# Performance work log

Measured on AMD Instinct MI355X. Metric: run time of the kernel, lower is better.

## Reference

```python
import jax, jax.numpy as jnp
import numpy as np

B, K, T, H, D = 16, 49, 256, 512, 512


def setup_inputs() -> dict:
    key = jax.random.key(0)
    ks = jax.random.split(key, 8)
    s = 1.0 / np.sqrt(H)
    return {
        "V": jax.random.normal(ks[0], (B, K, H), jnp.float32),
        "h_t": jax.random.normal(ks[1], (B, T, H), jnp.float32),
        "s_t": jax.random.normal(ks[2], (B, T, H), jnp.float32),
        "Wv": jax.random.normal(ks[3], (H, D), jnp.float32) * s,
        "bv": jnp.zeros((D,), jnp.float32),
        "Wg": jax.random.normal(ks[4], (H, D), jnp.float32) * s,
        "bg": jnp.zeros((D,), jnp.float32),
        "Ws": jax.random.normal(ks[5], (H, D), jnp.float32) * s,
        "bs": jnp.zeros((D,), jnp.float32),
        "Wh": jax.random.normal(ks[6], (D, 1), jnp.float32) * (1.0 / np.sqrt(D)),
        "bh": jnp.zeros((1,), jnp.float32),
    }


def reference(V, h_t, s_t, Wv, bv, Wg, bg, Ws, bs, Wh, bh):
    # projections (dropout is identity in eval)
    cv = V @ Wv + bv                        # [B, K, D]
    cg = h_t @ Wg + bg                      # [B, T, D]
    # content_v: [B, T, K, D] via broadcast add
    content_v = cv[:, None, :, :] + cg[:, :, None, :]
    z_t = (jnp.tanh(content_v) @ Wh + bh)[..., 0]   # [B, T, K]
    alpha_t = jax.nn.softmax(z_t, axis=-1)          # [B, T, K]
    c_t = jnp.einsum('btk,bkh->bth', alpha_t, V)    # [B, T, H]
    # sentinel branch
    content_s = (s_t @ Ws + bs) + cg                # [B, T, D]
    z_ext = jnp.tanh(content_s) @ Wh + bh           # [B, T, 1]
    extended = jnp.concatenate([z_t, z_ext], axis=-1)  # [B, T, K+1]
    alpha_hat = jax.nn.softmax(extended, axis=-1)
    beta_t = alpha_hat[:, :, -1:]                   # [B, T, 1]
    c_hat_t = beta_t * s_t + (1.0 - beta_t) * c_t   # [B, T, H]
    return (c_hat_t, alpha_t, beta_t)
```

## Files before the change

kernel.cpp:

```cpp
#include <hip/hip_runtime.h>
#include <hip/hip_fp16.h>
#include <cstdint>
#include <cstddef>

#define B_ 16
#define K_ 49
#define T_ 256
#define H_ 512
#define D_ 512

#define TANH_SCALE 2.8853900817779268f
#define LOG2E 1.4426950408889634f

typedef _Float16 half8 __attribute__((ext_vector_type(8)));
typedef float floatx4 __attribute__((ext_vector_type(4)));

#define ROWS_A 9088
#define OFF_V 0
#define OFF_H 896
#define OFF_S 4992

__device__ __forceinline__ void async16(const _Float16* g, const _Float16* l) {
    __builtin_amdgcn_global_load_lds(
        (const __attribute__((address_space(1))) unsigned int*)g,
        (__attribute__((address_space(3))) unsigned int*)l, 16, 0, 0);
}

__global__ __launch_bounds__(256) void conv_all(const float* __restrict__ V,
                                                const float* __restrict__ h_t,
                                                const float* __restrict__ s_t,
                                                const float* __restrict__ Wv,
                                                const float* __restrict__ Wg,
                                                const float* __restrict__ Ws,
                                                _Float16* __restrict__ Af16,
                                                _Float16* __restrict__ Wt) {
    __shared__ float tile[32][33];
    int tid = threadIdx.x;
    if (blockIdx.x < 2272) {
        int idx = (blockIdx.x * 256 + tid) * 8;
        int row = idx >> 9;
        int col = idx & 511;
        const float* src;
        if (row < 784)        src = V   + (size_t)row * 512 + col;
        else if (row < 896)   src = nullptr;
        else if (row < 4992)  src = h_t + (size_t)(row - 896) * 512 + col;
        else                  src = s_t + (size_t)(row - 4992) * 512 + col;
        half8 h;
        if (src) {
            float4 f0 = *(const float4*)(src);
            float4 f1 = *(const float4*)(src + 4);
            h[0] = (_Float16)f0.x; h[1] = (_Float16)f0.y;
            h[2] = (_Float16)f0.z; h[3] = (_Float16)f0.w;
            h[4] = (_Float16)f1.x; h[5] = (_Float16)f1.y;
            h[6] = (_Float16)f1.z; h[7] = (_Float16)f1.w;
        } else {
            h = (half8)((_Float16)0.0f);
        }
        *(half8*)(Af16 + idx) = h;
    } else {
        int bid = blockIdx.x - 2272;
        int p = bid >> 8;
        int rem = bid & 255;
        int bx = rem & 15, by = rem >> 4;
        const float* W = (p == 0) ? Wv : (p == 1) ? Wg : Ws;
        _Float16* outp = Wt + (size_t)p * 512 * 512;
        int tx = tid & 31, ty = tid >> 5;
        int c = bx * 32 + tx;
        int rbase = by * 32;
#pragma unroll
        for (int i = 0; i < 4; i++)
            tile[ty + i * 8][tx] = W[(size_t)(rbase + ty + i * 8) * 512 + c];
        __syncthreads();
        int k = rbase + tx;
#pragma unroll
        for (int i = 0; i < 4; i++) {
            int n = bx * 32 + ty + i * 8;
            outp[(size_t)n * 512 + k] = (_Float16)(tile[tx][ty + i * 8] * TANH_SCALE);
        }
    }
}

__global__ __launch_bounds__(256) void gemm_f16(
    const _Float16* __restrict__ Af16, const _Float16* __restrict__ Wt,
    const float* __restrict__ bv, const float* __restrict__ bg2,
    const float* __restrict__ bs, float* __restrict__ cv,
    float* __restrict__ cg, float* __restrict__ cs) {
    __shared__ __align__(16) _Float16 As[64 * 64];
    __shared__ __align__(16) _Float16 Bs[128 * 64];

    int id = blockIdx.x;
    int rowbase; const _Float16* Bt; const float* bias; float* C;
    if (id < 56)        { rowbase = OFF_V;            Bt = Wt;          bias = bv;  C = cv; }
    else if (id < 312)  { id -= 56;  rowbase = OFF_H; Bt = Wt + 262144; bias = bg2; C = cg; }
    else                { id -= 312; rowbase = OFF_S; Bt = Wt + 524288; bias = bs;  C = cs; }
    int tm = id >> 2, tn = id & 3;

    int tid = threadIdx.x;
    int wave = tid >> 6, lane = tid & 63;

    const _Float16* gA[2];
    int ldsA[2];
#pragma unroll
    for (int i = 0; i < 2; i++) {
        int p = i * 256 + tid;
        int ks = p >> 8, x = (p >> 6) & 3, q = (p >> 4) & 3, fm = p & 15;
        gA[i] = Af16 + (size_t)(rowbase + tm * 64 + x * 16 + fm) * 512 + ks * 32 + q * 8;
        ldsA[i] = p * 8;
    }
    const _Float16* gB[4];
    int ldsB[4];
#pragma unroll
    for (int i = 0; i < 4; i++) {
        int p = i * 256 + tid;
        int ks = p >> 9, w2y = (p >> 6) & 7, q = (p >> 4) & 3, fn = p & 15;
        gB[i] = Bt + (size_t)(tn * 128 + w2y * 16 + fn) * 512 + ks * 32 + q * 8;
        ldsB[i] = p * 8;
    }

    floatx4 acc[4][2];
#pragma unroll
    for (int x = 0; x < 4; x++)
#pragma unroll
        for (int y = 0; y < 2; y++) acc[x][y] = (floatx4)0.0f;

    for (int kk = 0; kk < 8; kk++) {
        if (kk) __syncthreads();
#pragma unroll
        for (int i = 0; i < 2; i++) async16(gA[i] + kk * 64, &As[ldsA[i]]);
#pragma unroll
        for (int i = 0; i < 4; i++) async16(gB[i] + kk * 64, &Bs[ldsB[i]]);
        __syncthreads();

#pragma unroll
        for (int ks = 0; ks < 2; ks++) {
            half8 a[4], bf[2];
#pragma unroll
            for (int x = 0; x < 4; x++)
                a[x] = *(const half8*)&As[((ks * 4 + x) * 64 + lane) * 8];
#pragma unroll
            for (int y = 0; y < 2; y++)
                bf[y] = *(const half8*)&Bs[((ks * 8 + wave * 2 + y) * 64 + lane) * 8];
#pragma unroll
            for (int x = 0; x < 4; x++)
#pragma unroll
                for (int y = 0; y < 2; y++)
                    acc[x][y] = __builtin_amdgcn_mfma_f32_16x16x32_f16(a[x], bf[y], acc[x][y], 0, 0, 0);
        }
    }

    int dn = lane & 15, dq = lane >> 4;
#pragma unroll
    for (int x = 0; x < 4; x++) {
        int rowg = tm * 64 + x * 16 + dq * 4;
#pragma unroll
        for (int y = 0; y < 2; y++) {
            int colg = tn * 128 + wave * 32 + y * 16 + dn;
            float bc = bias[colg] * TANH_SCALE;
#pragma unroll
            for (int r = 0; r < 4; r++)
                C[(size_t)(rowg + r) * 512 + colg] = acc[x][y][r] + bc;
        }
    }
}

__device__ __forceinline__ float wave_sum(float v) {
#pragma unroll
    for (int o = 32; o > 0; o >>= 1) v += __shfl_xor(v, o);
    return v;
}
__device__ __forceinline__ float wave_max(float v) {
#pragma unroll
    for (int o = 32; o > 0; o >>= 1) v = fmaxf(v, __shfl_xor(v, o));
    return v;
}

__device__ __forceinline__ float xsum4(float a0, float a1, float a2, float a3, int lane) {
    bool hi = (lane & 32) != 0;
    float t0 = hi ? a0 : a2;
    float t1 = hi ? a1 : a3;
    t0 = __shfl_xor(t0, 32);
    t1 = __shfl_xor(t1, 32);
    if (hi) { a0 = t0; a1 = t1; } else { a2 = t0; a3 = t1; }
    bool h2 = (lane & 16) != 0;
    float u0 = h2 ? a0 : a1;
    float u1 = h2 ? a2 : a3;
    u0 = __shfl_xor(u0, 16);
    u1 = __shfl_xor(u1, 16);
    if (h2) { a0 = u0; a2 = u1; } else { a1 = u0; a3 = u1; }
    float s = (a0 + a1) + (a2 + a3);
#pragma unroll
    for (int o = 8; o > 0; o >>= 1) s += __shfl_xor(s, o);
    return s;
}

#define TB 4
__global__ __launch_bounds__(256) void z_kernel(
    const float* __restrict__ cv, const float* __restrict__ cg,
    const float* __restrict__ cs, const float* __restrict__ V,
    const float* __restrict__ s_t, const float* __restrict__ Wh,
    const float* __restrict__ bh, float* __restrict__ out) {
    int bx = blockIdx.x;
    int b  = bx >> 6;
    int t0 = (bx & 63) << 2;
    int bt0 = b * 256 + t0;
    int tid = threadIdx.x;
    int wave = tid >> 6, lane = tid & 63;

    __shared__ float zl[TB][64];
    __shared__ float4 al4[52];
    __shared__ float bl[TB];

    float whv[8], egv[TB][8];
#pragma unroll
    for (int j = 0; j < 8; j++) whv[j] = Wh[j * 64 + lane];
#pragma unroll
    for (int tt = 0; tt < TB; tt++) {
        const float* cgp = cg + (size_t)(bt0 + tt) * 512;
#pragma unroll
        for (int j = 0; j < 8; j++)
            egv[tt][j] = __builtin_amdgcn_exp2f(cgp[j * 64 + lane]);
    }
    float s8 = 0.0f;
#pragma unroll
    for (int j = 0; j < 8; j++) s8 += whv[j];
    float zbase = wave_sum(s8) + bh[0];

    float rv[8], rn[8];
    {
        const float* rp = cv + (size_t)(b * 49 + wave) * 512;
#pragma unroll
        for (int j = 0; j < 8; j++) rv[j] = rp[j * 64 + lane];
    }
    for (int task = wave; task < 49; task += 4) {
        int nt = task + 4;
        if (nt < 49) {
            const float* rp = cv + (size_t)(b * 49 + nt) * 512;
#pragma unroll
            for (int j = 0; j < 8; j++) rn[j] = rp[j * 64 + lane];
        }
        float erv[8];
#pragma unroll
        for (int j = 0; j < 8; j++) erv[j] = __builtin_amdgcn_exp2f(rv[j]);
        float acc[TB] = {0.0f, 0.0f, 0.0f, 0.0f};
#pragma unroll
        for (int tt = 0; tt < TB; tt++) {
#pragma unroll
            for (int j = 0; j < 8; j++) {
                float e = erv[j] * egv[tt][j];
                float r = __builtin_amdgcn_rcpf(1.0f + e);
                acc[tt] = fmaf(whv[j], r, acc[tt]);
            }
        }
        float z = xsum4(acc[0], acc[1], acc[2], acc[3], lane);
        if ((lane & 15) == 0) zl[lane >> 4][task] = zbase - 2.0f * z;
#pragma unroll
        for (int j = 0; j < 8; j++) rv[j] = rn[j];
    }
#pragma unroll
    for (int tt = 0; tt < TB; tt++) {
        if (wave == tt) {
            const float* rp = cs + (size_t)(bt0 + tt) * 512;
            float acc = 0.0f;
#pragma unroll
            for (int j = 0; j < 8; j++) {
                float e = __builtin_amdgcn_exp2f(rp[j * 64 + lane]) * egv[tt][j];
                float r = __builtin_amdgcn_rcpf(1.0f + e);
                acc = fmaf(whv[j], r, acc);
            }
            float s = wave_sum(acc);
            if (lane == 0) zl[tt][49] = zbase - 2.0f * s;
        }
    }
    __syncthreads();

    {
        int w = wave;
        float z = (lane < 49) ? zl[w][lane] : -3.0e38f;
        float m = wave_max(z);
        float e = (lane < 49) ? __builtin_amdgcn_exp2f((z - m) * LOG2E) : 0.0f;
        float s = wave_sum(e);
        float zext = zl[w][49];
        float m2 = fmaxf(m, zext);
        float sc   = __builtin_amdgcn_exp2f((m - m2) * LOG2E);
        float eext = __builtin_amdgcn_exp2f((zext - m2) * LOG2E);
        float s2 = s * sc + eext;
        float beta = eext / s2;
        if (lane < 49) {
            float a = e / s;
            ((float*)&al4[lane])[w] = a;
            out[(size_t)B_ * T_ * H_ + (size_t)(bt0 + w) * 49 + lane] = a;
        }
        if (lane == 0) {
            bl[w] = beta;
            out[(size_t)B_ * T_ * H_ + (size_t)B_ * T_ * K_ + (bt0 + w)] = beta;
        }
    }
    __syncthreads();

    const float* Vb = V + (size_t)b * 49 * 512;
    float2 accA[TB];
#pragma unroll
    for (int tt = 0; tt < TB; tt++) accA[tt] = make_float2(0.0f, 0.0f);
#pragma unroll 7
    for (int k = 0; k < 49; k++) {
        float4 a4 = al4[k];
        float2 v = *(const float2*)(Vb + (size_t)k * 512 + tid * 2);
        accA[0].x = fmaf(a4.x, v.x, accA[0].x);  accA[0].y = fmaf(a4.x, v.y, accA[0].y);
        accA[1].x = fmaf(a4.y, v.x, accA[1].x);  accA[1].y = fmaf(a4.y, v.y, accA[1].y);
        accA[2].x = fmaf(a4.z, v.x, accA[2].x);  accA[2].y = fmaf(a4.z, v.y, accA[2].y);
        accA[3].x = fmaf(a4.w, v.x, accA[3].x);  accA[3].y = fmaf(a4.w, v.y, accA[3].y);
    }
#pragma unroll
    for (int tt = 0; tt < TB; tt++) {
        float beta = bl[tt];
        float2 sp = *(const float2*)(s_t + (size_t)(bt0 + tt) * 512 + tid * 2);
        float2 o;
        o.x = beta * sp.x + (1.0f - beta) * accA[tt].x;
        o.y = beta * sp.y + (1.0f - beta) * accA[tt].y;
        *(float2*)(out + (size_t)(bt0 + tt) * 512 + tid * 2) = o;
    }
}

extern "C" void kernel_launch(void* const* d_in, const int* in_sizes, int n_in,
                              void* d_out, int out_size, void* d_ws, size_t ws_size,
                              hipStream_t stream) {
    const float* V   = (const float*)d_in[0];
    const float* h_t = (const float*)d_in[1];
    const float* s_t = (const float*)d_in[2];
    const float* Wv  = (const float*)d_in[3];
    const float* bv  = (const float*)d_in[4];
    const float* Wg  = (const float*)d_in[5];
    const float* bg  = (const float*)d_in[6];
    const float* Ws  = (const float*)d_in[7];
    const float* bs  = (const float*)d_in[8];
    const float* Wh  = (const float*)d_in[9];
    const float* bh  = (const float*)d_in[10];
    float* out = (float*)d_out;

    char* ws = (char*)d_ws;
    _Float16* Af16 = (_Float16*)(ws);
    _Float16* Wt   = (_Float16*)(ws + 9306112);
    float* cv = (float*)(ws + 10878976);
    float* cg = (float*)(ws + 12713984);
    float* cs = (float*)(ws + 21102592);

    conv_all<<<3040, 256, 0, stream>>>(V, h_t, s_t, Wv, Wg, Ws, Af16, Wt);
    gemm_f16<<<568, 256, 0, stream>>>(Af16, Wt, bv, bg, bs, cv, cg, cs);
    z_kernel<<<1024, 256, 0, stream>>>(cv, cg, cs, V, s_t, Wh, bh, out);
}
```

Measured before the change: 135.6 us.

## Move exp2 into GEMM epilogue and shrink GEMM N-tile to 64

The GEMM epilogue now stores exp2 of the scaled projections, so z_kernel reads precomputed exponentials and forms 1+e with a single fma. This removes the per-tile recomputation of exp2 on cv rows, which z_kernel repeated for every time block. The GEMM tile also shrinks from 64x128 to 64x64 per block, doubling the grid to 1136 blocks for better CU occupancy, at the cost of lower per-block operand reuse. A risk is that exp2 of large pre-activations can overflow to inf, though rcp(1+inf) still gives the correct tanh limit.

```diff
diff --git a/kernel.cpp b/kernel.cpp
--- a/kernel.cpp
+++ b/kernel.cpp
@@ -86,80 +86,64 @@
     const float* __restrict__ bs, float* __restrict__ cv,
     float* __restrict__ cg, float* __restrict__ cs) {
     __shared__ __align__(16) _Float16 As[64 * 64];
-    __shared__ __align__(16) _Float16 Bs[128 * 64];
+    __shared__ __align__(16) _Float16 Bs[64 * 64];
 
     int id = blockIdx.x;
     int rowbase; const _Float16* Bt; const float* bias; float* C;
-    if (id < 56)        { rowbase = OFF_V;            Bt = Wt;          bias = bv;  C = cv; }
-    else if (id < 312)  { id -= 56;  rowbase = OFF_H; Bt = Wt + 262144; bias = bg2; C = cg; }
-    else                { id -= 312; rowbase = OFF_S; Bt = Wt + 524288; bias = bs;  C = cs; }
-    int tm = id >> 2, tn = id & 3;
+    if (id < 112)       { rowbase = OFF_V;            Bt = Wt;          bias = bv;  C = cv; }
+    else if (id < 624)  { id -= 112; rowbase = OFF_H; Bt = Wt + 262144; bias = bg2; C = cg; }
+    else                { id -= 624; rowbase = OFF_S; Bt = Wt + 524288; bias = bs;  C = cs; }
+    int tm = id >> 3, tn = id & 7;
 
     int tid = threadIdx.x;
     int wave = tid >> 6, lane = tid & 63;
 
-    const _Float16* gA[2];
-    int ldsA[2];
+    const _Float16* gA[2]; int ldsA[2];
+    const _Float16* gB[2]; int ldsB[2];
 #pragma unroll
     for (int i = 0; i < 2; i++) {
         int p = i * 256 + tid;
-        int ks = p >> 8, x = (p >> 6) & 3, q = (p >> 4) & 3, fm = p & 15;
-        gA[i] = Af16 + (size_t)(rowbase + tm * 64 + x * 16 + fm) * 512 + ks * 32 + q * 8;
+        int ks = p >> 8, x = (p >> 6) & 3, q = (p >> 4) & 3, f = p & 15;
+        gA[i] = Af16 + (size_t)(rowbase + tm * 64 + x * 16 + f) * 512 + ks * 32 + q * 8;
+        gB[i] = Bt   + (size_t)(tn * 64 + x * 16 + f) * 512 + ks * 32 + q * 8;
         ldsA[i] = p * 8;
-    }
-    const _Float16* gB[4];
-    int ldsB[4];
-#pragma unroll
-    for (int i = 0; i < 4; i++) {
-        int p = i * 256 + tid;
-        int ks = p >> 9, w2y = (p >> 6) & 7, q = (p >> 4) & 3, fn = p & 15;
-        gB[i] = Bt + (size_t)(tn * 128 + w2y * 16 + fn) * 512 + ks * 32 + q * 8;
         ldsB[i] = p * 8;
     }
 
-    floatx4 acc[4][2];
-#pragma unroll
-    for (int x = 0; x < 4; x++)
-#pragma unroll
-        for (int y = 0; y < 2; y++) acc[x][y] = (floatx4)0.0f;
+    floatx4 acc[4];
+#pragma unroll
+    for (int x = 0; x < 4; x++) acc[x] = (floatx4)0.0f;
 
     for (int kk = 0; kk < 8; kk++) {
         if (kk) __syncthreads();
 #pragma unroll
         for (int i = 0; i < 2; i++) async16(gA[i] + kk * 64, &As[ldsA[i]]);
 #pragma unroll
-        for (int i = 0; i < 4; i++) async16(gB[i] + kk * 64, &Bs[ldsB[i]]);
+        for (int i = 0; i < 2; i++) async16(gB[i] + kk * 64, &Bs[ldsB[i]]);
         __syncthreads();
 
 #pragma unroll
         for (int ks = 0; ks < 2; ks++) {
-            half8 a[4], bf[2];
+            half8 a[4];
 #pragma unroll
             for (int x = 0; x < 4; x++)
-                a[x] = *(const half8*)&As[((ks * 4 + x) * 64 + lane) * 8];
-#pragma unroll
-            for (int y = 0; y < 2; y++)
-                bf[y] = *(const half8*)&Bs[((ks * 8 + wave * 2 + y) * 64 + lane) * 8];
+                a[x] = *(const half8*)&As[(ks * 256 + x * 64 + lane) * 8];
+            half8 b = *(const half8*)&Bs[(ks * 256 + wave * 64 + lane) * 8];
 #pragma unroll
             for (int x = 0; x < 4; x++)
-#pragma unroll
-                for (int y = 0; y < 2; y++)
-                    acc[x][y] = __builtin_amdgcn_mfma_f32_16x16x32_f16(a[x], bf[y], acc[x][y], 0, 0, 0);
+                acc[x] = __builtin_amdgcn_mfma_f32_16x16x32_f16(a[x], b, acc[x], 0, 0, 0);
         }
     }
 
     int dn = lane & 15, dq = lane >> 4;
+    int colg = tn * 64 + wave * 16 + dn;
+    float bc = bias[colg] * TANH_SCALE;
 #pragma unroll
     for (int x = 0; x < 4; x++) {
         int rowg = tm * 64 + x * 16 + dq * 4;
 #pragma unroll
-        for (int y = 0; y < 2; y++) {
-            int colg = tn * 128 + wave * 32 + y * 16 + dn;
-            float bc = bias[colg] * TANH_SCALE;
-#pragma unroll
-            for (int r = 0; r < 4; r++)
-                C[(size_t)(rowg + r) * 512 + colg] = acc[x][y][r] + bc;
-        }
+        for (int r = 0; r < 4; r++)
+            C[(size_t)(rowg + r) * 512 + colg] = __builtin_amdgcn_exp2f(acc[x][r] + bc);
     }
 }
 
@@ -195,8 +179,8 @@
 
 #define TB 4
 __global__ __launch_bounds__(256) void z_kernel(
-    const float* __restrict__ cv, const float* __restrict__ cg,
-    const float* __restrict__ cs, const float* __restrict__ V,
+    const float* __restrict__ ecv, const float* __restrict__ ecg,
+    const float* __restrict__ ecs, const float* __restrict__ V,
     const float* __restrict__ s_t, const float* __restrict__ Wh,
     const float* __restrict__ bh, float* __restrict__ out) {
     int bx = blockIdx.x;
@@ -215,10 +199,9 @@
     for (int j = 0; j < 8; j++) whv[j] = Wh[j * 64 + lane];
 #pragma unroll
     for (int tt = 0; tt < TB; tt++) {
-        const float* cgp = cg + (size_t)(bt0 + tt) * 512;
-#pragma unroll
-        for (int j = 0; j < 8; j++)
-            egv[tt][j] = __builtin_amdgcn_exp2f(cgp[j * 64 + lane]);
+        const float* cgp = ecg + (size_t)(bt0 + tt) * 512;
+#pragma unroll
+        for (int j = 0; j < 8; j++) egv[tt][j] = cgp[j * 64 + lane];
     }
     float s8 = 0.0f;
 #pragma unroll
@@ -227,27 +210,24 @@
 
     float rv[8], rn[8];
     {
-        const float* rp = cv + (size_t)(b * 49 + wave) * 512;
+        const float* rp = ecv + (size_t)(b * 49 + wave) * 512;
 #pragma unroll
         for (int j = 0; j < 8; j++) rv[j] = rp[j * 64 + lane];
     }
     for (int task = wave; task < 49; task += 4) {
         int nt = task + 4;
         if (nt < 49) {
-            const float* rp = cv + (size_t)(b * 49 + nt) * 512;
+            const float* rp = ecv + (size_t)(b * 49 + nt) * 512;
 #pragma unroll
             for (int j = 0; j < 8; j++) rn[j] = rp[j * 64 + lane];
         }
-        float erv[8];
-#pragma unroll
-        for (int j = 0; j < 8; j++) erv[j] = __builtin_amdgcn_exp2f(rv[j]);
         float acc[TB] = {0.0f, 0.0f, 0.0f, 0.0f};
 #pragma unroll
         for (int tt = 0; tt < TB; tt++) {
 #pragma unroll
             for (int j = 0; j < 8; j++) {
-                float e = erv[j] * egv[tt][j];
-                float r = __builtin_amdgcn_rcpf(1.0f + e);
+                float t = fmaf(rv[j], egv[tt][j], 1.0f);
+                float r = __builtin_amdgcn_rcpf(t);
                 acc[tt] = fmaf(whv[j], r, acc[tt]);
             }
         }
@@ -259,12 +239,12 @@
 #pragma unroll
     for (int tt = 0; tt < TB; tt++) {
         if (wave == tt) {
-            const float* rp = cs + (size_t)(bt0 + tt) * 512;
+            const float* rp = ecs + (size_t)(bt0 + tt) * 512;
             float acc = 0.0f;
 #pragma unroll
             for (int j = 0; j < 8; j++) {
-                float e = __builtin_amdgcn_exp2f(rp[j * 64 + lane]) * egv[tt][j];
-                float r = __builtin_amdgcn_rcpf(1.0f + e);
+                float t = fmaf(rp[j * 64 + lane], egv[tt][j], 1.0f);
+                float r = __builtin_amdgcn_rcpf(t);
                 acc = fmaf(whv[j], r, acc);
             }
             float s = wave_sum(acc);
@@ -340,11 +320,11 @@
     char* ws = (char*)d_ws;
     _Float16* Af16 = (_Float16*)(ws);
     _Float16* Wt   = (_Float16*)(ws + 9306112);
-    float* cv = (float*)(ws + 10878976);
-    float* cg = (float*)(ws + 12713984);
-    float* cs = (float*)(ws + 21102592);
+    float* ecv = (float*)(ws + 10878976);
+    float* ecg = (float*)(ws + 12713984);
+    float* ecs = (float*)(ws + 21102592);
 
     conv_all<<<3040, 256, 0, stream>>>(V, h_t, s_t, Wv, Wg, Ws, Af16, Wt);
-    gemm_f16<<<568, 256, 0, stream>>>(Af16, Wt, bv, bg, bs, cv, cg, cs);
-    z_kernel<<<1024, 256, 0, stream>>>(cv, cg, cs, V, s_t, Wh, bh, out);
-}
+    gemm_f16<<<1136, 256, 0, stream>>>(Af16, Wt, bv, bg, bs, ecv, ecg, ecs);
+    z_kernel<<<1024, 256, 0, stream>>>(ecv, ecg, ecs, V, s_t, Wh, bh, out);
+}
```

After: 135.1 us. No clear change (-0.4%).
